# Performance work log

Measured on AMD Instinct MI355X. Metric: run time of the kernel, lower is better.

The kernel has to match this reference:

```python
import jax, jax.numpy as jnp
import numpy as np

N = 1024  # step_num
M = 1024  # state_num
C = 64    # in_channels


def _mlp3(x, w1, b1, w2, b2, w3, b3):
    # LinearStack(3, C, C, out): Linear+ReLU, Linear+ReLU, Linear
    h = jax.nn.relu(x @ w1 + b1)
    h = jax.nn.relu(h @ w2 + b2)
    return h @ w3 + b3


def setup_inputs() -> dict:
    key = jax.random.key(0)
    ks = jax.random.split(key, 10)
    s = 1.0 / np.sqrt(C)
    return {
        'step_x': jax.random.normal(ks[0], (N, C), jnp.float32),
        'state_x': jax.random.normal(ks[1], (M, C), jnp.float32),
        'pre_w1': jax.random.normal(ks[2], (C, C), jnp.float32) * s,
        'pre_b1': jnp.zeros((C,), jnp.float32),
        'pre_w2': jax.random.normal(ks[3], (C, C), jnp.float32) * s,
        'pre_b2': jnp.zeros((C,), jnp.float32),
        'pre_w3': jax.random.normal(ks[4], (C, C), jnp.float32) * s,
        'pre_b3': jnp.zeros((C,), jnp.float32),
        'post_w1': jax.random.normal(ks[5], (C, C), jnp.float32) * s,
        'post_b1': jnp.zeros((C,), jnp.float32),
        'post_w2': jax.random.normal(ks[6], (C, C), jnp.float32) * s,
        'post_b2': jnp.zeros((C,), jnp.float32),
        'post_w3': jax.random.normal(ks[7], (C, 2), jnp.float32) * s,
        'post_b3': jnp.zeros((2,), jnp.float32),
    }


def reference(step_x, state_x,
              pre_w1, pre_b1, pre_w2, pre_b2, pre_w3, pre_b3,
              post_w1, post_b1, post_w2, post_b2, post_w3, post_b3):
    # pre-compare MLP on both node sets
    sx = _mlp3(step_x, pre_w1, pre_b1, pre_w2, pre_b2, pre_w3, pre_b3)   # [N,C]
    tx = _mlp3(state_x, pre_w1, pre_b1, pre_w2, pre_b2, pre_w3, pre_b3)  # [M,C]
    n, c = sx.shape
    m = tx.shape[0]

    # step-step pairwise compare ('add') + post-compare -> [N,N,2]
    pair_ss = (sx[:, None, :] + sx[None, :, :]).reshape(n * n, c)
    logits_ss = _mlp3(pair_ss, post_w1, post_b1, post_w2, post_b2,
                      post_w3, post_b3).reshape(n, n, 2)

    # step-state pairwise compare + post-compare -> [N,M,2]
    pair_st = (sx[:, None, :] + tx[None, :, :]).reshape(n * m, c)
    logits_st = _mlp3(pair_st, post_w1, post_b1, post_w2, post_b2,
                      post_w3, post_b3).reshape(n, m, 2)

    # mutual-argmax bipartite matching on sigmoid(match logits)
    match = jax.nn.sigmoid(logits_st[..., 0])                 # [N,M]
    col_arg = jnp.argmax(match, axis=0)                       # [M]
    mask_c = (jnp.arange(n)[:, None] == col_arg[None, :]).astype(match.dtype)
    s1 = match * mask_c
    row_arg = jnp.argmax(s1, axis=1)                          # [N]
    mask_r = (jnp.arange(m)[None, :] == row_arg[:, None]).astype(s1.dtype)
    matched_scores = s1 * mask_r                              # [N,M]

    return logits_ss, logits_st, matched_scores
```

## Files before the change

kernel.cpp:

```cpp
#include <hip/hip_runtime.h>
#include <math.h>

namespace {

constexpr int N_ = 1024;
constexpr int M_ = 1024;
constexpr int C_ = 64;

typedef _Float16 f16x8 __attribute__((ext_vector_type(8)));
typedef float f32x4 __attribute__((ext_vector_type(4)));
static_assert(sizeof(f16x8) == 16, "f16x8 must be 4 VGPRs");

__device__ __forceinline__ float sig(float x) { return 1.0f / (1.0f + expf(-x)); }

__device__ __forceinline__ unsigned flipbits(float f) {
    unsigned u = __float_as_uint(f);
    return u ^ (0x80000000u | (unsigned)((int)u >> 31));
}
__device__ __forceinline__ float unflipbits(unsigned k) {
    unsigned u = (k & 0x80000000u) ? (k ^ 0x80000000u) : ~k;
    return __uint_as_float(u);
}
__device__ __forceinline__ unsigned long long packlogit(float v, unsigned idx) {
    return ((unsigned long long)flipbits(v) << 32) | (unsigned)(0xFFFFFFFFu - idx);
}
__device__ __forceinline__ unsigned long long packpos(float v, unsigned idx) {
    return ((unsigned long long)__float_as_uint(v) << 32) | (unsigned)(0xFFFFFFFFu - idx);
}

__global__ __launch_bounds__(256) void pre_prep_kernel(
    const float* __restrict__ step_x, const float* __restrict__ state_x,
    const float* __restrict__ w1, const float* __restrict__ b1,
    const float* __restrict__ w2, const float* __restrict__ b2,
    const float* __restrict__ w3, const float* __restrict__ b3,
    const float* __restrict__ pw1, const float* __restrict__ pw2,
    float* __restrict__ U, _Float16* __restrict__ w2T)
{
    const int t = threadIdx.x;
    if (blockIdx.x == 128) {
        for (int e = t; e < C_ * C_; e += 256) {
            int k = e >> 6, c = e & 63;
            w2T[c * 64 + k] = (_Float16)pw2[e];
        }
        return;
    }

    __shared__ float XA[16][C_ + 1];
    __shared__ float XB[16][C_ + 1];
    __shared__ float W[C_ * C_];
    __shared__ float Bv[C_];

    const int c = t & 63;
    const int rg = t >> 6;
    const int rbase = blockIdx.x * 16;

    const float* src_g = (rbase < N_) ? (step_x + (size_t)rbase * C_)
                                      : (state_x + (size_t)(rbase - N_) * C_);
    {
        int row = t >> 4, k4 = (t & 15) << 2;
        float4 v = *reinterpret_cast<const float4*>(src_g + row * C_ + k4);
        XA[row][k4 + 0] = v.x; XA[row][k4 + 1] = v.y;
        XA[row][k4 + 2] = v.z; XA[row][k4 + 3] = v.w;
    }

    const float* Ws[4] = {w1, w2, w3, pw1};
    const float* Bs[4] = {b1, b2, b3, nullptr};

    float (*sA)[C_ + 1] = XA;
    float (*sB)[C_ + 1] = XB;

    for (int layer = 0; layer < 4; ++layer) {
        __syncthreads();
        for (int e = t; e < C_ * C_ / 4; e += 256)
            reinterpret_cast<float4*>(W)[e] =
                reinterpret_cast<const float4*>(Ws[layer])[e];
        if (t < C_) Bv[t] = (layer == 3) ? 0.0f : Bs[layer][t];
        __syncthreads();
        const bool relu = (layer < 2);
        #pragma unroll
        for (int q = 0; q < 4; ++q) {
            const int row = rg * 4 + q;
            float acc = Bv[c];
            #pragma unroll 8
            for (int k = 0; k < C_; ++k)
                acc = fmaf(sA[row][k], W[k * C_ + c], acc);
            sB[row][c] = relu ? fmaxf(acc, 0.0f) : acc;
        }
        float (*tmp)[C_ + 1] = sA; sA = sB; sB = tmp;
    }
    #pragma unroll
    for (int q = 0; q < 4; ++q) {
        const int row = rg * 4 + q;
        U[(size_t)(rbase + row) * C_ + c] = sA[row][c];
    }
}

__global__ __launch_bounds__(256) void pair_kernel(
    const float* __restrict__ U,
    const _Float16* __restrict__ w2T,
    const float* __restrict__ pb1, const float* __restrict__ pb2,
    const float* __restrict__ pw3, const float* __restrict__ pb3,
    float* __restrict__ out)
{
    __shared__ float SU[32][68];
    __shared__ float SVB[32][68];
    __shared__ float OUTT[32][33][2];

    const int t = threadIdx.x;
    const int lane = t & 63;
    const int wave = t >> 6;
    const int wi = wave >> 1, wj = wave & 1;
    const int zz = blockIdx.z;
    const int ibase = blockIdx.y * 32;
    const int jbase = blockIdx.x * 32;

    {
        int r = t >> 3, k0 = (t & 7) * 8;
        const float* up = U + (size_t)(ibase + r) * C_ + k0;
        *reinterpret_cast<float4*>(&SU[r][k0])     = *reinterpret_cast<const float4*>(up);
        *reinterpret_cast<float4*>(&SU[r][k0 + 4]) = *reinterpret_cast<const float4*>(up + 4);
        const float* vp = U + (size_t)((zz ? N_ : 0) + jbase + r) * C_ + k0;
        float4 b0 = *reinterpret_cast<const float4*>(vp);
        float4 b1v = *reinterpret_cast<const float4*>(vp + 4);
        float4 c0 = *reinterpret_cast<const float4*>(pb1 + k0);
        float4 c1 = *reinterpret_cast<const float4*>(pb1 + k0 + 4);
        b0.x += c0.x; b0.y += c0.y; b0.z += c0.z; b0.w += c0.w;
        b1v.x += c1.x; b1v.y += c1.y; b1v.z += c1.z; b1v.w += c1.w;
        *reinterpret_cast<float4*>(&SVB[r][k0])     = b0;
        *reinterpret_cast<float4*>(&SVB[r][k0 + 4]) = b1v;
    }

    const int ch_l = lane & 15;
    const int kg = lane >> 4;

    f16x8 whi[4][2];
    #pragma unroll
    for (int mt = 0; mt < 4; ++mt)
        #pragma unroll
        for (int ks = 0; ks < 2; ++ks)
            whi[mt][ks] = *reinterpret_cast<const f16x8*>(
                w2T + (mt * 16 + ch_l) * 64 + ks * 32 + kg * 8);

    float b2v[16], w30[16], w31[16];
    #pragma unroll
    for (int mt = 0; mt < 4; ++mt)
        #pragma unroll
        for (int r = 0; r < 4; ++r) {
            int ch = mt * 16 + kg * 4 + r;
            b2v[mt * 4 + r] = pb2[ch];
            w30[mt * 4 + r] = pw3[ch * 2];
            w31[mt * 4 + r] = pw3[ch * 2 + 1];
        }
    const float ob0 = pb3[0], ob1 = pb3[1];

    __syncthreads();

    float su[2][8];
    #pragma unroll
    for (int ks = 0; ks < 2; ++ks) {
        int k0 = ks * 32 + kg * 8;
        float4 a = *reinterpret_cast<const float4*>(&SU[wi * 16 + ch_l][k0]);
        float4 b = *reinterpret_cast<const float4*>(&SU[wi * 16 + ch_l][k0 + 4]);
        su[ks][0] = a.x; su[ks][1] = a.y; su[ks][2] = a.z; su[ks][3] = a.w;
        su[ks][4] = b.x; su[ks][5] = b.y; su[ks][6] = b.z; su[ks][7] = b.w;
    }

    for (int jj = 0; jj < 16; ++jj) {
        const int jr = wj * 16 + jj;
        f16x8 bhi[2];
        #pragma unroll
        for (int ks = 0; ks < 2; ++ks) {
            int k0 = ks * 32 + kg * 8;
            float4 a = *reinterpret_cast<const float4*>(&SVB[jr][k0]);
            float4 b = *reinterpret_cast<const float4*>(&SVB[jr][k0 + 4]);
            float sv[8] = {a.x, a.y, a.z, a.w, b.x, b.y, b.z, b.w};
            #pragma unroll
            for (int e = 0; e < 8; ++e)
                bhi[ks][e] = (_Float16)fmaxf(su[ks][e] + sv[e], 0.0f);
        }
        f32x4 ah[4];
        #pragma unroll
        for (int mt = 0; mt < 4; ++mt)
            ah[mt] = f32x4{b2v[4 * mt], b2v[4 * mt + 1], b2v[4 * mt + 2], b2v[4 * mt + 3]};
        #pragma unroll
        for (int ks = 0; ks < 2; ++ks)
            #pragma unroll
            for (int mt = 0; mt < 4; ++mt)
                ah[mt] = __builtin_amdgcn_mfma_f32_16x16x32_f16(whi[mt][ks], bhi[ks], ah[mt], 0, 0, 0);
        float p0 = 0.0f, p1 = 0.0f;
        #pragma unroll
        for (int mt = 0; mt < 4; ++mt)
            #pragma unroll
            for (int r = 0; r < 4; ++r) {
                float g = fmaxf(ah[mt][r], 0.0f);
                p0 = fmaf(g, w30[4 * mt + r], p0);
                p1 = fmaf(g, w31[4 * mt + r], p1);
            }
        p0 += __shfl_xor(p0, 16); p0 += __shfl_xor(p0, 32);
        p1 += __shfl_xor(p1, 16); p1 += __shfl_xor(p1, 32);
        if (lane < 16) {
            OUTT[wi * 16 + lane][wj * 16 + jj][0] = p0 + ob0;
            OUTT[wi * 16 + lane][wj * 16 + jj][1] = p1 + ob1;
        }
    }
    __syncthreads();
    {
        float* obase = out + (size_t)zz * (2ull * N_ * M_);
        int r = t >> 3;
        int q0 = (t & 7) * 4;
        int i = ibase + r;
        #pragma unroll
        for (int q = 0; q < 4; ++q) {
            int j = jbase + q0 + q;
            float2 v = *reinterpret_cast<float2*>(&OUTT[r][q0 + q][0]);
            *reinterpret_cast<float2*>(obase + ((size_t)i * M_ + j) * 2) = v;
        }
    }
}

__global__ __launch_bounds__(256) void colmax1_kernel(
    const float* __restrict__ Lst, unsigned long long* __restrict__ PT2)
{
    int j = blockIdx.x * 256 + threadIdx.x;
    int ic = blockIdx.y;
    unsigned long long k1 = 0, k2 = 0;
    for (int q = 0; q < 32; ++q) {
        int i = ic * 32 + q;
        unsigned long long k = packlogit(Lst[((size_t)i * M_ + j) * 2], (unsigned)i);
        if (k > k1) { k2 = k1; k1 = k; } else if (k > k2) k2 = k;
    }
    PT2[((size_t)ic * M_ + j) * 2]     = k1;
    PT2[((size_t)ic * M_ + j) * 2 + 1] = k2;
}

__global__ __launch_bounds__(128) void colmax2_kernel(
    const unsigned long long* __restrict__ PT2,
    int2* __restrict__ colinfo, unsigned long long* __restrict__ rowbest)
{
    int j = blockIdx.x * 128 + threadIdx.x;
    unsigned long long k1 = 0, k2 = 0;
    for (int ic = 0; ic < 32; ++ic) {
        unsigned long long a = PT2[((size_t)ic * M_ + j) * 2];
        unsigned long long b = PT2[((size_t)ic * M_ + j) * 2 + 1];
        if (a > k1) { k2 = k1; k1 = a; } else if (a > k2) k2 = a;
        if (b > k1) { k2 = k1; k1 = b; } else if (b > k2) k2 = b;
    }
    int i1 = (int)(0xFFFFFFFFu - (unsigned)(k1 & 0xFFFFFFFFull));
    int i2 = (int)(0xFFFFFFFFu - (unsigned)(k2 & 0xFFFFFFFFull));
    float v1 = unflipbits((unsigned)(k1 >> 32));
    float v2 = unflipbits((unsigned)(k2 >> 32));
    int2 info; info.x = i1; info.y = (v1 - v2 < 8e-3f) ? i2 : -1;
    colinfo[j] = info;
    rowbest[j] = 0ull;
}

__global__ __launch_bounds__(64) void exactvals_kernel(
    const float* __restrict__ U, const float* __restrict__ pb1,
    const float* __restrict__ pw2, const float* __restrict__ pb2,
    const float* __restrict__ pw3, const float* __restrict__ pb3,
    const int2* __restrict__ colinfo, unsigned long long* __restrict__ rowbest)
{
    __shared__ float h1s[64];
    int j = blockIdx.x;
    int lane = threadIdx.x;
    int2 info = colinfo[j];
    int ids[2] = {info.x, info.y};
    int nc = (info.y >= 0) ? 2 : 1;
    float logits[2] = {0.0f, 0.0f};
    for (int cnd = 0; cnd < nc; ++cnd) {
        int i = ids[cnd];
        h1s[lane] = fmaxf(U[(size_t)i * C_ + lane] + U[(size_t)(N_ + j) * C_ + lane] + pb1[lane], 0.0f);
        __syncthreads();
        float acc = pb2[lane];
        #pragma unroll 8
        for (int k = 0; k < 64; ++k)
            acc = fmaf(h1s[k], pw2[k * 64 + lane], acc);
        float p = fmaxf(acc, 0.0f) * pw3[lane * 2];
        #pragma unroll
        for (int m = 1; m < 64; m <<= 1) p += __shfl_xor(p, m);
        logits[cnd] = p + pb3[0];
        __syncthreads();
    }
    int wi; float wp;
    if (nc == 1) { wi = ids[0]; wp = logits[0]; }
    else if (logits[0] > logits[1]) { wi = ids[0]; wp = logits[0]; }
    else if (logits[1] > logits[0]) { wi = ids[1]; wp = logits[1]; }
    else { wi = min(ids[0], ids[1]); wp = logits[0]; }
    if (lane == 0)
        atomicMax(&rowbest[wi], packpos(sig(wp), (unsigned)j));
}

__global__ __launch_bounds__(256) void zscatter_kernel(
    const unsigned long long* __restrict__ rowbest, float* __restrict__ matched)
{
    int i = blockIdx.x;
    int t = threadIdx.x;
    *reinterpret_cast<float4*>(matched + (size_t)i * M_ + t * 4) =
        float4{0.0f, 0.0f, 0.0f, 0.0f};
    __syncthreads();
    if (t == 0) {
        unsigned long long key = rowbest[i];
        if (key) {
            unsigned j = 0xFFFFFFFFu - (unsigned)(key & 0xFFFFFFFFull);
            matched[(size_t)i * M_ + j] = __uint_as_float((unsigned)(key >> 32));
        }
    }
}

}

extern "C" void kernel_launch(void* const* d_in, const int* in_sizes, int n_in,
                              void* d_out, int out_size, void* d_ws, size_t ws_size,
                              hipStream_t stream)
{
    const float* step_x  = (const float*)d_in[0];
    const float* state_x = (const float*)d_in[1];
    const float* pre_w1  = (const float*)d_in[2];
    const float* pre_b1  = (const float*)d_in[3];
    const float* pre_w2  = (const float*)d_in[4];
    const float* pre_b2  = (const float*)d_in[5];
    const float* pre_w3  = (const float*)d_in[6];
    const float* pre_b3  = (const float*)d_in[7];
    const float* post_w1 = (const float*)d_in[8];
    const float* post_b1 = (const float*)d_in[9];
    const float* post_w2 = (const float*)d_in[10];
    const float* post_b2 = (const float*)d_in[11];
    const float* post_w3 = (const float*)d_in[12];
    const float* post_b3 = (const float*)d_in[13];

    float* out     = (float*)d_out;
    float* Lst     = out + 2ull * N_ * M_;
    float* matched = out + 4ull * N_ * M_;

    float* U = (float*)d_ws;
    unsigned long long* rowbest = (unsigned long long*)((char*)d_ws + 2048ull * 64 * 4);

    char* ms = (char*)matched;
    unsigned long long* PT2 = (unsigned long long*)ms;
    int2*      colinfo = (int2*)(ms + 512 * 1024);
    _Float16*  w2T     = (_Float16*)(ms + 520 * 1024);

    hipLaunchKernelGGL(pre_prep_kernel, dim3(129), dim3(256), 0, stream,
        step_x, state_x, pre_w1, pre_b1, pre_w2, pre_b2, pre_w3, pre_b3,
        post_w1, post_w2, U, w2T);
    hipLaunchKernelGGL(pair_kernel, dim3(32, 32, 2), dim3(256), 0, stream,
        U, w2T, post_b1, post_b2, post_w3, post_b3, out);
    hipLaunchKernelGGL(colmax1_kernel, dim3(4, 32), dim3(256), 0, stream,
        Lst, PT2);
    hipLaunchKernelGGL(colmax2_kernel, dim3(8), dim3(128), 0, stream,
        PT2, colinfo, rowbest);
    hipLaunchKernelGGL(exactvals_kernel, dim3(1024), dim3(64), 0, stream,
        U, post_b1, post_w2, post_b2, post_w3, post_b3, colinfo, rowbest);
    hipLaunchKernelGGL(zscatter_kernel, dim3(1024), dim3(256), 0, stream,
        rowbest, matched);
}
```

Baseline: 158.2 us.

## Fuse column top-2 reduction into pair kernel and merge final colmax

The per-tile column top-2 reduction over match logits now happens inside pair_kernel from the shared-memory output tile, so the separate colmax1 pass no longer re-reads the step-state logits from global memory. colmax2 is merged into the exact-value kernel through a wave-level shuffle reduction, and rowbest zeroing moves into pre_prep, together removing two launches. The fp16 packing of the hidden pair activations also switches to packed cvt_pkrtz conversions, which use round-toward-zero instead of round-to-nearest. The cost is extra shared memory and a few block barriers in the z=1 blocks of pair_kernel.

```diff
diff --git a/kernel.cpp b/kernel.cpp
--- a/kernel.cpp
+++ b/kernel.cpp
@@ -8,6 +8,7 @@
 constexpr int C_ = 64;
 
 typedef _Float16 f16x8 __attribute__((ext_vector_type(8)));
+typedef __fp16 fp16x2 __attribute__((ext_vector_type(2)));
 typedef float f32x4 __attribute__((ext_vector_type(4)));
 static_assert(sizeof(f16x8) == 16, "f16x8 must be 4 VGPRs");
 
@@ -26,6 +27,11 @@
 }
 __device__ __forceinline__ unsigned long long packpos(float v, unsigned idx) {
     return ((unsigned long long)__float_as_uint(v) << 32) | (unsigned)(0xFFFFFFFFu - idx);
+}
+__device__ __forceinline__ unsigned long long shflx64(unsigned long long v, int m) {
+    unsigned lo = __shfl_xor((unsigned)v, m);
+    unsigned hi = __shfl_xor((unsigned)(v >> 32), m);
+    return ((unsigned long long)hi << 32) | lo;
 }
 
 __global__ __launch_bounds__(256) void pre_prep_kernel(
@@ -34,7 +40,8 @@
     const float* __restrict__ w2, const float* __restrict__ b2,
     const float* __restrict__ w3, const float* __restrict__ b3,
     const float* __restrict__ pw1, const float* __restrict__ pw2,
-    float* __restrict__ U, _Float16* __restrict__ w2T)
+    float* __restrict__ U, _Float16* __restrict__ w2T,
+    unsigned long long* __restrict__ rowbest)
 {
     const int t = threadIdx.x;
     if (blockIdx.x == 128) {
@@ -42,6 +49,7 @@
             int k = e >> 6, c = e & 63;
             w2T[c * 64 + k] = (_Float16)pw2[e];
         }
+        for (int e = t; e < 1024; e += 256) rowbest[e] = 0ull;
         return;
     }
 
@@ -100,11 +108,12 @@
     const _Float16* __restrict__ w2T,
     const float* __restrict__ pb1, const float* __restrict__ pb2,
     const float* __restrict__ pw3, const float* __restrict__ pb3,
-    float* __restrict__ out)
+    float* __restrict__ out, unsigned long long* __restrict__ PT2)
 {
     __shared__ float SU[32][68];
     __shared__ float SVB[32][68];
     __shared__ float OUTT[32][33][2];
+    __shared__ unsigned long long RED[8][32][2];
 
     const int t = threadIdx.x;
     const int lane = t & 63;
@@ -174,9 +183,14 @@
             float4 a = *reinterpret_cast<const float4*>(&SVB[jr][k0]);
             float4 b = *reinterpret_cast<const float4*>(&SVB[jr][k0 + 4]);
             float sv[8] = {a.x, a.y, a.z, a.w, b.x, b.y, b.z, b.w};
+            union { f16x8 v; fp16x2 h2[4]; } bu;
             #pragma unroll
-            for (int e = 0; e < 8; ++e)
-                bhi[ks][e] = (_Float16)fmaxf(su[ks][e] + sv[e], 0.0f);
+            for (int m = 0; m < 4; ++m) {
+                float x0 = fmaxf(su[ks][2 * m]     + sv[2 * m],     0.0f);
+                float x1 = fmaxf(su[ks][2 * m + 1] + sv[2 * m + 1], 0.0f);
+                bu.h2[m] = __builtin_amdgcn_cvt_pkrtz(x0, x1);
+            }
+            bhi[ks] = bu.v;
         }
         f32x4 ah[4];
         #pragma unroll
@@ -216,56 +230,58 @@
             *reinterpret_cast<float2*>(obase + ((size_t)i * M_ + j) * 2) = v;
         }
     }
-}
-
-__global__ __launch_bounds__(256) void colmax1_kernel(
-    const float* __restrict__ Lst, unsigned long long* __restrict__ PT2)
-{
-    int j = blockIdx.x * 256 + threadIdx.x;
-    int ic = blockIdx.y;
-    unsigned long long k1 = 0, k2 = 0;
-    for (int q = 0; q < 32; ++q) {
-        int i = ic * 32 + q;
-        unsigned long long k = packlogit(Lst[((size_t)i * M_ + j) * 2], (unsigned)i);
-        if (k > k1) { k2 = k1; k1 = k; } else if (k > k2) k2 = k;
-    }
-    PT2[((size_t)ic * M_ + j) * 2]     = k1;
-    PT2[((size_t)ic * M_ + j) * 2 + 1] = k2;
-}
-
-__global__ __launch_bounds__(128) void colmax2_kernel(
+    if (zz) {
+        const int tc = t & 31, tg = t >> 5;
+        unsigned long long k1 = 0, k2 = 0;
+        #pragma unroll
+        for (int q = 0; q < 4; ++q) {
+            int r = tg * 4 + q;
+            unsigned long long k = packlogit(OUTT[r][tc][0], (unsigned)(ibase + r));
+            if (k > k1) { k2 = k1; k1 = k; } else if (k > k2) k2 = k;
+        }
+        RED[tg][tc][0] = k1; RED[tg][tc][1] = k2;
+        for (int h = 4; h > 0; h >>= 1) {
+            __syncthreads();
+            if (tg < h) {
+                unsigned long long a = RED[tg + h][tc][0], b = RED[tg + h][tc][1];
+                if (a > k1) { k2 = k1; k1 = a; } else if (a > k2) k2 = a;
+                if (b > k1) { k2 = k1; k1 = b; } else if (b > k2) k2 = b;
+                RED[tg][tc][0] = k1; RED[tg][tc][1] = k2;
+            }
+        }
+        if (tg == 0) {
+            size_t o = ((size_t)blockIdx.y * M_ + (jbase + tc)) * 2;
+            PT2[o] = k1; PT2[o + 1] = k2;
+        }
+    }
+}
+
+__global__ __launch_bounds__(64) void colfinal_kernel(
     const unsigned long long* __restrict__ PT2,
-    int2* __restrict__ colinfo, unsigned long long* __restrict__ rowbest)
-{
-    int j = blockIdx.x * 128 + threadIdx.x;
-    unsigned long long k1 = 0, k2 = 0;
-    for (int ic = 0; ic < 32; ++ic) {
-        unsigned long long a = PT2[((size_t)ic * M_ + j) * 2];
-        unsigned long long b = PT2[((size_t)ic * M_ + j) * 2 + 1];
-        if (a > k1) { k2 = k1; k1 = a; } else if (a > k2) k2 = a;
-        if (b > k1) { k2 = k1; k1 = b; } else if (b > k2) k2 = b;
-    }
-    int i1 = (int)(0xFFFFFFFFu - (unsigned)(k1 & 0xFFFFFFFFull));
-    int i2 = (int)(0xFFFFFFFFu - (unsigned)(k2 & 0xFFFFFFFFull));
-    float v1 = unflipbits((unsigned)(k1 >> 32));
-    float v2 = unflipbits((unsigned)(k2 >> 32));
-    int2 info; info.x = i1; info.y = (v1 - v2 < 8e-3f) ? i2 : -1;
-    colinfo[j] = info;
-    rowbest[j] = 0ull;
-}
-
-__global__ __launch_bounds__(64) void exactvals_kernel(
     const float* __restrict__ U, const float* __restrict__ pb1,
     const float* __restrict__ pw2, const float* __restrict__ pb2,
     const float* __restrict__ pw3, const float* __restrict__ pb3,
-    const int2* __restrict__ colinfo, unsigned long long* __restrict__ rowbest)
+    unsigned long long* __restrict__ rowbest)
 {
     __shared__ float h1s[64];
-    int j = blockIdx.x;
-    int lane = threadIdx.x;
-    int2 info = colinfo[j];
-    int ids[2] = {info.x, info.y};
-    int nc = (info.y >= 0) ? 2 : 1;
+    const int j = blockIdx.x;
+    const int lane = threadIdx.x;
+
+    unsigned long long k1 = PT2[((size_t)(lane >> 1) * M_ + j) * 2 + (lane & 1)];
+    unsigned long long k2 = 0;
+    #pragma unroll
+    for (int m = 1; m < 64; m <<= 1) {
+        unsigned long long a = shflx64(k1, m), b = shflx64(k2, m);
+        if (a > k1) { k2 = k1; k1 = a; } else if (a > k2) k2 = a;
+        if (b > k1) { k2 = k1; k1 = b; } else if (b > k2) k2 = b;
+    }
+    int ids[2];
+    ids[0] = (int)(0xFFFFFFFFu - (unsigned)(k1 & 0xFFFFFFFFull));
+    ids[1] = (int)(0xFFFFFFFFu - (unsigned)(k2 & 0xFFFFFFFFull));
+    float v1 = unflipbits((unsigned)(k1 >> 32));
+    float v2 = unflipbits((unsigned)(k2 >> 32));
+    const int nc = (v1 - v2 < 8e-3f) ? 2 : 1;
+
     float logits[2] = {0.0f, 0.0f};
     for (int cnd = 0; cnd < nc; ++cnd) {
         int i = ids[cnd];
@@ -329,7 +345,6 @@
     const float* post_b3 = (const float*)d_in[13];
 
     float* out     = (float*)d_out;
-    float* Lst     = out + 2ull * N_ * M_;
     float* matched = out + 4ull * N_ * M_;
 
     float* U = (float*)d_ws;
@@ -337,20 +352,15 @@
 
     char* ms = (char*)matched;
     unsigned long long* PT2 = (unsigned long long*)ms;
-    int2*      colinfo = (int2*)(ms + 512 * 1024);
-    _Float16*  w2T     = (_Float16*)(ms + 520 * 1024);
+    _Float16*  w2T     = (_Float16*)(ms + 512 * 1024);
 
     hipLaunchKernelGGL(pre_prep_kernel, dim3(129), dim3(256), 0, stream,
         step_x, state_x, pre_w1, pre_b1, pre_w2, pre_b2, pre_w3, pre_b3,
-        post_w1, post_w2, U, w2T);
+        post_w1, post_w2, U, w2T, rowbest);
     hipLaunchKernelGGL(pair_kernel, dim3(32, 32, 2), dim3(256), 0, stream,
-        U, w2T, post_b1, post_b2, post_w3, post_b3, out);
-    hipLaunchKernelGGL(colmax1_kernel, dim3(4, 32), dim3(256), 0, stream,
-        Lst, PT2);
-    hipLaunchKernelGGL(colmax2_kernel, dim3(8), dim3(128), 0, stream,
-        PT2, colinfo, rowbest);
-    hipLaunchKernelGGL(exactvals_kernel, dim3(1024), dim3(64), 0, stream,
-        U, post_b1, post_w2, post_b2, post_w3, post_b3, colinfo, rowbest);
+        U, w2T, post_b1, post_b2, post_w3, post_b3, out, PT2);
+    hipLaunchKernelGGL(colfinal_kernel, dim3(1024), dim3(64), 0, stream,
+        PT2, U, post_b1, post_w2, post_b2, post_w3, post_b3, rowbest);
     hipLaunchKernelGGL(zscatter_kernel, dim3(1024), dim3(256), 0, stream,
         rowbest, matched);
 }
```

Result: faster. 147.2 us (-6.9%).
